# Performance work log

Hardware: AMD Instinct MI355X
Metric: run time of the kernel (lower is better)

Reference implementation:

```python
import jax, jax.numpy as jnp
import numpy as np

B, T, D, H, HD = 2, 2048, 1024, 16, 64
EPS = 1.1920929e-07  # torch.finfo(float32).eps used by F.rms_norm default
VE_GATE_SCALE = 2.0
KEY_OFFSET = True


def rms_norm(x):
    return x * jax.lax.rsqrt(jnp.mean(x * x, axis=-1, keepdims=True) + EPS)


def apply_rotary(x, cos, sin):
    # x: [B,T,H,HD], cos/sin: [T, HD//2]
    c = cos[None, :, None, :]
    s = sin[None, :, None, :]
    x1, x2 = jnp.split(x, 2, axis=-1)
    return jnp.concatenate([x1 * c + x2 * s, -x1 * s + x2 * c], axis=-1)


def setup_inputs() -> dict:
    key = jax.random.key(0)
    ks = jax.random.split(key, 8)
    bound = (3.0 ** 0.5) * (D ** -0.5)
    x = jax.random.normal(ks[0], (B, T, D), dtype=jnp.float32)
    ve = jax.random.normal(ks[1], (B, T, H * HD), dtype=jnp.float32)
    sa_lambdas = jnp.ones((2,), dtype=jnp.float32)
    # realistic RoPE tables
    inv_freq = (10000.0 ** (-np.arange(HD // 2) / (HD // 2))).astype(np.float32)
    ang = np.arange(T, dtype=np.float32)[:, None] * inv_freq[None, :]
    cos = jnp.asarray(np.cos(ang))
    sin = jnp.asarray(np.sin(ang))
    # qkvo weight: uniform init everywhere (orig zeros o-proj; randomized for a non-trivial baseline)
    qkvo_w = jax.random.uniform(ks[2], (4 * D, D), dtype=jnp.float32, minval=-bound, maxval=bound)
    attn_gate_w = 0.02 * jax.random.normal(ks[3], (H, D), dtype=jnp.float32)
    ve_gate_w = 0.02 * jax.random.normal(ks[4], (H, D), dtype=jnp.float32)
    attn_scale = jnp.float32(0.12)
    docs = jnp.sort(jax.random.randint(ks[5], (T,), 0, 8).astype(jnp.int32))
    return {"x": x, "ve": ve, "sa_lambdas": sa_lambdas, "cos": cos, "sin": sin,
            "qkvo_w": qkvo_w, "attn_gate_w": attn_gate_w, "ve_gate_w": ve_gate_w,
            "attn_scale": attn_scale, "docs": docs}


def reference(x, ve, sa_lambdas, cos, sin, qkvo_w, attn_gate_w, ve_gate_w, attn_scale, docs):
    # QKV projection: rows [0:3D] of qkvo_w
    qkv = jnp.einsum('btd,ed->bte', x, sa_lambdas[0] * qkvo_w[:3 * D])
    qkv = qkv.reshape(B, T, 3 * H, HD)
    q, k, v = qkv[:, :, :H], qkv[:, :, H:2 * H], qkv[:, :, 2 * H:]
    q, k = rms_norm(q), rms_norm(k)
    q, k = apply_rotary(q, cos, sin), apply_rotary(k, cos, sin)
    if KEY_OFFSET:
        # shift two head-dim bands of k forward by one position
        k = k.at[:, 1:, :, HD // 4:HD // 2].set(k[:, :-1, :, HD // 4:HD // 2])
        k = k.at[:, 1:, :, 3 * HD // 4:].set(k[:, :-1, :, 3 * HD // 4:])
    # gated value embedding
    ve_gate = VE_GATE_SCALE * jax.nn.sigmoid(jnp.einsum('btd,hd->bth', x, ve_gate_w))
    v = v + ve_gate[..., None] * ve.reshape(B, T, H, HD)
    # causal + document masked attention (score_mod semantics)
    idx = jnp.arange(T)
    mask = (idx[:, None] >= idx[None, :]) & (docs[:, None] == docs[None, :])  # [T,T]
    scores = jnp.einsum('bqhd,bkhd->bhqk', q, k) * attn_scale
    scores = jnp.where(mask[None, None], scores, -jnp.inf)
    p = jax.nn.softmax(scores, axis=-1)
    y = jnp.einsum('bhqk,bkhd->bqhd', p, v)
    # attention output gate
    attn_gate = jax.nn.sigmoid(jnp.einsum('btd,hd->bth', x, attn_gate_w))
    y = y * attn_gate[..., None]
    # output projection: rows [3D:4D]
    y = y.reshape(B, T, H * HD)
    out = jnp.einsum('btd,ed->bte', y, sa_lambdas[1] * qkvo_w[3 * D:])
    return out
```

## Files before the change

### kernel.cpp

```cpp
#include <hip/hip_runtime.h>
#include <math.h>

#define B_ 2
#define T_ 2048
#define D_ 1024
#define H_ 16
#define HD_ 64
#define EPS_ 1.1920929e-07f
#define VE_SCALE_ 2.0f

#define NX4_ (B_ * T_ * D_ / 4)
#define NS4_ (3 * D_ * D_ / 4)
#define NQ4_ (4 * D_ * D_ / 4)
#define NG4_ (H_ * D_ / 4)

typedef __bf16 bf16_t;
typedef __bf16 bf16x4 __attribute__((ext_vector_type(4)));
typedef __bf16 bf16x8 __attribute__((ext_vector_type(8)));
typedef float f32x4 __attribute__((ext_vector_type(4)));

__device__ const f32x4 F4ZERO = {0.f, 0.f, 0.f, 0.f};

typedef __attribute__((address_space(1))) const void gvoid_t;
typedef __attribute__((address_space(3))) void lvoid_t;

__device__ __forceinline__ void gl_lds16(const bf16_t* g, bf16_t* l) {
  __builtin_amdgcn_global_load_lds((gvoid_t*)g, (lvoid_t*)l, 16, 0, 0);
}

__global__ __launch_bounds__(256) void cast_all(
    const float* __restrict__ x, const float* __restrict__ qkvo,
    const float* __restrict__ agw, const float* __restrict__ vgw,
    bf16_t* __restrict__ x_bf, bf16_t* __restrict__ wq,
    bf16_t* __restrict__ wo, bf16_t* __restrict__ wg)
{
  const int i = blockIdx.x * 256 + threadIdx.x;
  const float4* src;
  bf16x4* dst;
  if (i < NX4_) {
    src = (const float4*)x + i;
    dst = (bf16x4*)x_bf + i;
  } else if (i < NX4_ + NS4_) {
    const int j = i - NX4_;
    src = (const float4*)qkvo + j;
    dst = (bf16x4*)wq + j;
  } else if (i < NX4_ + NQ4_) {
    const int j = i - NX4_;
    src = (const float4*)qkvo + j;
    dst = (bf16x4*)wo + (j - NS4_);
  } else if (i < NX4_ + NQ4_ + NG4_) {
    const int j = i - NX4_ - NQ4_;
    src = (const float4*)agw + j;
    dst = (bf16x4*)wg + j;
  } else {
    const int j = i - NX4_ - NQ4_ - NG4_;
    src = (const float4*)vgw + j;
    dst = (bf16x4*)wg + NG4_ + j;
  }
  const float4 v = *src;
  bf16x4 o = {(bf16_t)v.x, (bf16_t)v.y, (bf16_t)v.z, (bf16_t)v.w};
  *dst = o;
}

__global__ __launch_bounds__(256) void gemm_bf16(
    const bf16_t* __restrict__ A, const bf16_t* __restrict__ W,
    void* __restrict__ Cout, int M, int N, int K,
    const float* __restrict__ lam, int li, int out_bf)
{
  const float scale = lam[li];
  __shared__ bf16_t As[2][128][32];
  __shared__ bf16_t Bs[2][128][32];
  const int tid = threadIdx.x;
  const int lane = tid & 63, w = tid >> 6;
  const int lr = lane & 15, lg = lane >> 4;
  const int wr = w >> 1, wc = w & 1;

  const int nwg = gridDim.x * gridDim.y;
  int bid = blockIdx.y * gridDim.x + blockIdx.x;
  bid = (bid & 7) * (nwg >> 3) + (bid >> 3);
  const int row0 = (bid / gridDim.x) * 128;
  const int col0 = (bid % gridDim.x) * 128;

  const int srow = w * 32 + (lane >> 2);
  const int scol = (lane & 3) * 8;
  const bf16_t* Ag = A + (size_t)(row0 + srow) * K + scol;
  const bf16_t* Wg = W + (size_t)(col0 + srow) * K + scol;
  const size_t r16 = (size_t)16 * K;

  f32x4 acc[4][4];
#pragma unroll
  for (int i = 0; i < 4; ++i)
#pragma unroll
    for (int j = 0; j < 4; ++j) acc[i][j] = F4ZERO;

#define STAGE_(bi, kk)                                    \
  do {                                                    \
    gl_lds16(Ag + (kk), &As[bi][w * 32][0]);              \
    gl_lds16(Ag + r16 + (kk), &As[bi][w * 32 + 16][0]);   \
    gl_lds16(Wg + (kk), &Bs[bi][w * 32][0]);              \
    gl_lds16(Wg + r16 + (kk), &Bs[bi][w * 32 + 16][0]);   \
  } while (0)

#define COMPUTE_(bi)                                                     \
  do {                                                                   \
    bf16x8 af[4], bfr[4];                                                \
    _Pragma("unroll")                                                    \
    for (int fm = 0; fm < 4; ++fm)                                       \
      af[fm] = *(const bf16x8*)&As[bi][wr * 64 + fm * 16 + lr][lg * 8];  \
    _Pragma("unroll")                                                    \
    for (int fn = 0; fn < 4; ++fn)                                       \
      bfr[fn] = *(const bf16x8*)&Bs[bi][wc * 64 + fn * 16 + lr][lg * 8]; \
    _Pragma("unroll")                                                    \
    for (int fm = 0; fm < 4; ++fm)                                       \
      _Pragma("unroll")                                                  \
      for (int fn = 0; fn < 4; ++fn)                                     \
        acc[fm][fn] = __builtin_amdgcn_mfma_f32_16x16x32_bf16(           \
            af[fm], bfr[fn], acc[fm][fn], 0, 0, 0);                      \
  } while (0)

  STAGE_(0, 0);
  __syncthreads();
  for (int k0 = 0; k0 + 64 <= K; k0 += 64) {
    STAGE_(1, k0 + 32);
    COMPUTE_(0);
    __syncthreads();
    if (k0 + 64 < K) STAGE_(0, k0 + 64);
    COMPUTE_(1);
    __syncthreads();
  }
#undef STAGE_
#undef COMPUTE_

#pragma unroll
  for (int fm = 0; fm < 4; ++fm)
#pragma unroll
    for (int fn = 0; fn < 4; ++fn)
#pragma unroll
      for (int r = 0; r < 4; ++r) {
        const int row = row0 + wr * 64 + fm * 16 + lg * 4 + r;
        const int col = col0 + wc * 64 + fn * 16 + lr;
        const float v = acc[fm][fn][r] * scale;
        if (out_bf) ((bf16_t*)Cout)[(size_t)row * N + col] = (bf16_t)v;
        else        ((float*)Cout)[(size_t)row * N + col] = v;
      }
}

__global__ __launch_bounds__(256) void post_kernel(
    const float* __restrict__ x, const bf16_t* __restrict__ qkv_b,
    const float* __restrict__ ve, const float* __restrict__ cosb,
    const float* __restrict__ sinb, const bf16_t* __restrict__ wg,
    bf16_t* __restrict__ q_bf, bf16_t* __restrict__ k_bf,
    bf16_t* __restrict__ v_bf, float* __restrict__ attn_gate)
{
  const int bt = blockIdx.x;
  const int b = bt >> 11, t = bt & (T_ - 1);
  const int tid = threadIdx.x;
  __shared__ float xs[D_];
  __shared__ float gsc[32];

  *(float4*)&xs[tid * 4] = ((const float4*)(x + (size_t)bt * D_))[tid];
  __syncthreads();

  {
    const int g = tid >> 3, cg = tid & 7;
    const bf16x8* wrow = (const bf16x8*)(wg + (size_t)g * D_);
    float sum = 0.f;
#pragma unroll
    for (int j = 0; j < 16; ++j) {
      const bf16x8 w8 = wrow[cg + 8 * j];
      const float* xp = &xs[(cg + 8 * j) * 8];
#pragma unroll
      for (int e = 0; e < 8; ++e) sum = fmaf((float)w8[e], xp[e], sum);
    }
    sum += __shfl_xor(sum, 1);
    sum += __shfl_xor(sum, 2);
    sum += __shfl_xor(sum, 4);
    if (cg == 0)
      gsc[g] = (g < 16 ? 1.f : VE_SCALE_) / (1.f + __expf(-sum));
  }
  __syncthreads();

  const int w = tid >> 6, lane = tid & 63;
  const float c = cosb[t * 32 + (lane & 31)];
  const float s = sinb[t * 32 + (lane & 31)];
  const size_t row = (size_t)bt * 3072;
#pragma unroll
  for (int i = 0; i < 4; ++i) {
    const int h = w + i * 4;
    const float qraw = (float)qkv_b[row + h * HD_ + lane];
    const float kraw = (float)qkv_b[row + D_ + h * HD_ + lane];
    const float vraw = (float)qkv_b[row + 2 * D_ + h * HD_ + lane];
    float ssq = qraw * qraw, ssk = kraw * kraw;
#pragma unroll
    for (int off = 32; off > 0; off >>= 1) {
      ssq += __shfl_xor(ssq, off);
      ssk += __shfl_xor(ssk, off);
    }
    const float qn = qraw * rsqrtf(ssq * (1.f / 64.f) + EPS_);
    const float kn = kraw * rsqrtf(ssk * (1.f / 64.f) + EPS_);
    const float qpartner = __shfl_xor(qn, 32);
    const float kpartner = __shfl_xor(kn, 32);
    const float qo = (lane < 32) ? fmaf(qn, c, qpartner * s)
                                 : fmaf(qn, c, -qpartner * s);
    const float ko = (lane < 32) ? fmaf(kn, c, kpartner * s)
                                 : fmaf(kn, c, -kpartner * s);
    const size_t oidx = ((size_t)(b * H_ + h) * T_ + t) * HD_ + lane;
    q_bf[oidx] = (bf16_t)qo;
    k_bf[oidx] = (bf16_t)ko;
    const float vv = fmaf(gsc[16 + h], ve[(size_t)bt * D_ + h * HD_ + lane], vraw);
    v_bf[oidx] = (bf16_t)vv;
    if (lane == 0) attn_gate[bt * H_ + h] = gsc[h];
  }
}

__global__ __launch_bounds__(256) void attn_mfma(
    const bf16_t* __restrict__ q_buf, const bf16_t* __restrict__ k_tmp,
    const bf16_t* __restrict__ v_buf, const float* __restrict__ attn_gate,
    const int* __restrict__ docs, const float* __restrict__ scale_ptr,
    bf16_t* __restrict__ y_buf)
{
  const int qt = blockIdx.x, bh = blockIdx.y;
  const int b = bh >> 4, h = bh & 15;
  const int tid = threadIdx.x;
  const int w = tid >> 6, lane = tid & 63;
  const int lr = lane & 15, lg = lane >> 4;
  const float scale = scale_ptr[0];
  __shared__ bf16_t Ks[64][72];
  __shared__ bf16_t Vt[64][72];
  __shared__ bf16_t Ps[64][72];
  __shared__ int dk[64];

  const int dlo = docs[qt * 64];
  const unsigned long long bal =
      __ballot((lane <= qt) && (docs[lane * 64 + 63] >= dlo));
  const int ktlo = __ffsll(bal) - 1;

  const bf16_t* qp = q_buf + ((size_t)bh * T_ + qt * 64 + w * 16 + lr) * HD_;
  const bf16x8 aq0 = *(const bf16x8*)(qp + lg * 8);
  const bf16x8 aq1 = *(const bf16x8*)(qp + 32 + lg * 8);
  int qpos_r[4], docq_r[4];
#pragma unroll
  for (int r = 0; r < 4; ++r) {
    qpos_r[r] = qt * 64 + w * 16 + lg * 4 + r;
    docq_r[r] = docs[qpos_r[r]];
  }
  f32x4 acc[4];
#pragma unroll
  for (int fn = 0; fn < 4; ++fn) acc[fn] = F4ZERO;
  float m[4] = {-1e30f, -1e30f, -1e30f, -1e30f};
  float l[4] = {0.f, 0.f, 0.f, 0.f};

#pragma unroll 1
  for (int kt = ktlo; kt <= qt; ++kt) {
    __syncthreads();
#pragma unroll
    for (int i = 0; i < 2; ++i) {
      const int idx = i * 256 + tid;
      const int krow = idx >> 3;
      const int c8 = (idx & 7) << 3;
      const int gk = kt * 64 + krow;
      const int gks = (((c8 & 16) != 0) && gk > 0) ? gk - 1 : gk;
      *(bf16x8*)&Ks[krow][c8] =
          *(const bf16x8*)(k_tmp + ((size_t)bh * T_ + gks) * HD_ + c8);
      const int kpos = idx & 63;
      const int d0 = (idx >> 6) << 3;
      const bf16x8 vv =
          *(const bf16x8*)(v_buf + ((size_t)bh * T_ + kt * 64 + kpos) * HD_ + d0);
#pragma unroll
      for (int j = 0; j < 8; ++j) Vt[d0 + j][kpos] = vv[j];
    }
    if (tid < 64) dk[tid] = docs[kt * 64 + tid];
    __syncthreads();

    f32x4 s[4];
#pragma unroll
    for (int fn = 0; fn < 4; ++fn) {
      const bf16x8 bk0 = *(const bf16x8*)&Ks[fn * 16 + lr][lg * 8];
      const bf16x8 bk1 = *(const bf16x8*)&Ks[fn * 16 + lr][32 + lg * 8];
      f32x4 z = F4ZERO;
      z = __builtin_amdgcn_mfma_f32_16x16x32_bf16(aq0, bk0, z, 0, 0, 0);
      s[fn] = __builtin_amdgcn_mfma_f32_16x16x32_bf16(aq1, bk1, z, 0, 0, 0);
    }
    const bool strict = (kt < qt);
#pragma unroll
    for (int fn = 0; fn < 4; ++fn) {
      const int kd = dk[fn * 16 + lr];
      const int kp = kt * 64 + fn * 16 + lr;
#pragma unroll
      for (int r = 0; r < 4; ++r) {
        const bool valid = (kd == docq_r[r]) && (strict || kp <= qpos_r[r]);
        s[fn][r] = valid ? s[fn][r] * scale : -3.0e38f;
      }
    }
#pragma unroll
    for (int r = 0; r < 4; ++r) {
      float cm = fmaxf(fmaxf(s[0][r], s[1][r]), fmaxf(s[2][r], s[3][r]));
      cm = fmaxf(cm, __shfl_xor(cm, 1));
      cm = fmaxf(cm, __shfl_xor(cm, 2));
      cm = fmaxf(cm, __shfl_xor(cm, 4));
      cm = fmaxf(cm, __shfl_xor(cm, 8));
      const float mn = fmaxf(m[r], cm);
      const float sc = __expf(m[r] - mn);
      m[r] = mn;
      const float p0 = __expf(s[0][r] - mn);
      const float p1 = __expf(s[1][r] - mn);
      const float p2 = __expf(s[2][r] - mn);
      const float p3 = __expf(s[3][r] - mn);
      float ps = (p0 + p1) + (p2 + p3);
      ps += __shfl_xor(ps, 1);
      ps += __shfl_xor(ps, 2);
      ps += __shfl_xor(ps, 4);
      ps += __shfl_xor(ps, 8);
      l[r] = l[r] * sc + ps;
      acc[0][r] *= sc; acc[1][r] *= sc; acc[2][r] *= sc; acc[3][r] *= sc;
      const int prow = w * 16 + lg * 4 + r;
      Ps[prow][0 + lr]  = (bf16_t)p0;
      Ps[prow][16 + lr] = (bf16_t)p1;
      Ps[prow][32 + lr] = (bf16_t)p2;
      Ps[prow][48 + lr] = (bf16_t)p3;
    }
    const bf16x8 ap0 = *(const bf16x8*)&Ps[w * 16 + lr][lg * 8];
    const bf16x8 ap1 = *(const bf16x8*)&Ps[w * 16 + lr][32 + lg * 8];
#pragma unroll
    for (int fn = 0; fn < 4; ++fn) {
      const bf16x8 bv0 = *(const bf16x8*)&Vt[fn * 16 + lr][lg * 8];
      const bf16x8 bv1 = *(const bf16x8*)&Vt[fn * 16 + lr][32 + lg * 8];
      acc[fn] = __builtin_amdgcn_mfma_f32_16x16x32_bf16(ap0, bv0, acc[fn], 0, 0, 0);
      acc[fn] = __builtin_amdgcn_mfma_f32_16x16x32_bf16(ap1, bv1, acc[fn], 0, 0, 0);
    }
  }
#pragma unroll
  for (int r = 0; r < 4; ++r) {
    const float inv = attn_gate[(size_t)(b * T_ + qpos_r[r]) * H_ + h] / l[r];
#pragma unroll
    for (int fn = 0; fn < 4; ++fn)
      y_buf[(size_t)(b * T_ + qpos_r[r]) * D_ + h * HD_ + fn * 16 + lr] =
          (bf16_t)(acc[fn][r] * inv);
  }
}

extern "C" void kernel_launch(void* const* d_in, const int* in_sizes, int n_in,
                              void* d_out, int out_size, void* d_ws, size_t ws_size,
                              hipStream_t stream) {
  const float* x    = (const float*)d_in[0];
  const float* ve   = (const float*)d_in[1];
  const float* lam  = (const float*)d_in[2];
  const float* cosb = (const float*)d_in[3];
  const float* sinb = (const float*)d_in[4];
  const float* qkvo = (const float*)d_in[5];
  const float* agw  = (const float*)d_in[6];
  const float* vgw  = (const float*)d_in[7];
  const float* ascl = (const float*)d_in[8];
  const int*   docs = (const int*)d_in[9];
  float* out = (float*)d_out;

  const size_t BT = (size_t)B_ * T_;
  float* cur = (float*)d_ws;
  bf16_t* x_bf = (bf16_t*)cur;        cur += BT * D_ / 2;
  bf16_t* wq_bf = (bf16_t*)cur;       cur += (size_t)3 * D_ * D_ / 2;
  bf16_t* wo_bf = (bf16_t*)cur;       cur += (size_t)D_ * D_ / 2;
  bf16_t* wg_bf = (bf16_t*)cur;       cur += (size_t)2 * H_ * D_ / 2;
  bf16_t* qkv_b = (bf16_t*)cur;       cur += BT * 3 * D_ / 2;
  bf16_t* q_bf = (bf16_t*)cur;        cur += BT * D_ / 2;
  bf16_t* k_bf = (bf16_t*)cur;        cur += BT * D_ / 2;
  bf16_t* v_bf = (bf16_t*)cur;        cur += BT * D_ / 2;
  bf16_t* y_bf = (bf16_t*)cur;        cur += BT * D_ / 2;
  float* attn_gate = cur;             cur += BT * H_;

  cast_all<<<(NX4_ + NQ4_ + 2 * NG4_) / 256, 256, 0, stream>>>(
      x, qkvo, agw, vgw, x_bf, wq_bf, wo_bf, wg_bf);

  gemm_bf16<<<dim3(3 * D_ / 128, BT / 128), 256, 0, stream>>>(
      x_bf, wq_bf, qkv_b, (int)BT, 3 * D_, D_, lam, 0, 1);

  post_kernel<<<(int)BT, 256, 0, stream>>>(
      x, qkv_b, ve, cosb, sinb, wg_bf, q_bf, k_bf, v_bf, attn_gate);

  attn_mfma<<<dim3(T_ / 64, B_ * H_), 256, 0, stream>>>(
      q_bf, k_bf, v_bf, attn_gate, docs, ascl, y_bf);

  gemm_bf16<<<dim3(D_ / 128, BT / 128), 256, 0, stream>>>(
      y_bf, wo_bf, out, (int)BT, D_, D_, lam, 1, 0);
}
```

Before: 131.3 us.

## Add 256x256 tiled bf16 GEMM with phased pipelining for QKV projection

```diff
diff --git a/kernel.cpp b/kernel.cpp
--- a/kernel.cpp
+++ b/kernel.cpp
@@ -62,6 +62,122 @@
   *dst = o;
 }
 
+__global__ __launch_bounds__(512, 2) void gemm256(
+    const bf16_t* __restrict__ A, const bf16_t* __restrict__ W,
+    void* __restrict__ Cout, int M, int N, int K,
+    const float* __restrict__ lam, int li, int out_bf)
+{
+  __shared__ bf16_t As[2][256][64];
+  __shared__ bf16_t Bs[2][256][64];
+  const float scale = lam[li];
+  const int tid = threadIdx.x;
+  const int w = tid >> 6, lane = tid & 63;
+  const int lr = lane & 15, lg = lane >> 4;
+  const int wr = w >> 2, wc = w & 3;
+  const int sw = lr & 7;
+
+  const int nwg = gridDim.x * gridDim.y;
+  int bid = blockIdx.y * gridDim.x + blockIdx.x;
+  bid = (bid & 7) * (nwg >> 3) + (bid >> 3);
+  const int row0 = (bid / gridDim.x) * 256;
+  const int col0 = (bid % gridDim.x) * 256;
+
+  const int arow0 = (w & 3) * 8 + ((w >> 2) ? 128 : 0);
+  const int srow = arow0 + (lane >> 3);
+  const int sgran = (lane & 7) ^ ((lane >> 3) & 7);
+  const bf16_t* Abase = A + (size_t)(row0 + srow) * K + sgran * 8;
+  const bf16_t* Wbase = W + (size_t)(col0 + srow) * K + sgran * 8;
+
+#define STA(buf, j, kk) gl_lds16(Abase + (size_t)((j) * 32) * K + (kk), \
+                                 &As[buf][arow0 + (j) * 32][0])
+#define STB(buf, j, kk) gl_lds16(Wbase + (size_t)((j) * 32) * K + (kk), \
+                                 &Bs[buf][arow0 + (j) * 32][0])
+#define LDA(buf, fm, kh) \
+  (*(const bf16x8*)&As[buf][wr * 128 + (fm) * 16 + lr][((((kh) * 4) + lg) ^ sw) * 8])
+#define LDB(buf, fn, kh) \
+  (*(const bf16x8*)&Bs[buf][wc * 64 + (fn) * 16 + lr][((((kh) * 4) + lg) ^ sw) * 8])
+
+  f32x4 acc[8][4];
+#pragma unroll
+  for (int i = 0; i < 8; ++i)
+#pragma unroll
+    for (int j = 0; j < 4; ++j) acc[i][j] = F4ZERO;
+  bf16x8 bb[4][2];
+
+#define PH(vm, q, cur, ISSUE)                                                  \
+  do {                                                                         \
+    asm volatile("s_waitcnt vmcnt(" #vm ")" ::: "memory");                     \
+    __builtin_amdgcn_s_barrier();                                              \
+    if ((q) == 0) {                                                            \
+      _Pragma("unroll") for (int fn = 0; fn < 4; ++fn) {                       \
+        bb[fn][0] = LDB(cur, fn, 0);                                           \
+        bb[fn][1] = LDB(cur, fn, 1);                                           \
+      }                                                                        \
+    }                                                                          \
+    bf16x8 a00 = LDA(cur, 2 * (q), 0), a01 = LDA(cur, 2 * (q), 1);             \
+    bf16x8 a10 = LDA(cur, 2 * (q) + 1, 0), a11 = LDA(cur, 2 * (q) + 1, 1);     \
+    ISSUE;                                                                     \
+    asm volatile("s_waitcnt lgkmcnt(0)" ::: "memory");                         \
+    __builtin_amdgcn_sched_barrier(0);                                         \
+    __builtin_amdgcn_s_setprio(1);                                             \
+    _Pragma("unroll") for (int fn = 0; fn < 4; ++fn) {                         \
+      acc[2 * (q)][fn] = __builtin_amdgcn_mfma_f32_16x16x32_bf16(              \
+          a00, bb[fn][0], acc[2 * (q)][fn], 0, 0, 0);                          \
+      acc[2 * (q)][fn] = __builtin_amdgcn_mfma_f32_16x16x32_bf16(              \
+          a01, bb[fn][1], acc[2 * (q)][fn], 0, 0, 0);                          \
+      acc[2 * (q) + 1][fn] = __builtin_amdgcn_mfma_f32_16x16x32_bf16(          \
+          a10, bb[fn][0], acc[2 * (q) + 1][fn], 0, 0, 0);                      \
+      acc[2 * (q) + 1][fn] = __builtin_amdgcn_mfma_f32_16x16x32_bf16(          \
+          a11, bb[fn][1], acc[2 * (q) + 1][fn], 0, 0, 0);                      \
+    }                                                                          \
+    __builtin_amdgcn_s_setprio(0);                                             \
+    __builtin_amdgcn_s_barrier();                                              \
+  } while (0)
+
+  STB(0, 0, 0); STB(0, 1, 0); STB(0, 2, 0); STB(0, 3, 0);
+  STA(0, 0, 0); STA(0, 1, 0); STA(0, 2, 0); STA(0, 3, 0);
+
+  const int nt = K >> 6;
+  int kt = 0;
+  for (; kt < nt - 1; ++kt) {
+    const int kn = (kt + 1) << 6;
+    if ((kt & 1) == 0) {
+      PH(3, 0, 0, { STB(1, 0, kn); STB(1, 1, kn); });
+      PH(4, 1, 0, { STB(1, 2, kn); STB(1, 3, kn); });
+      PH(5, 2, 0, { STA(1, 0, kn); STA(1, 1, kn); });
+      PH(6, 3, 0, { STA(1, 2, kn); STA(1, 3, kn); });
+    } else {
+      PH(3, 0, 1, { STB(0, 0, kn); STB(0, 1, kn); });
+      PH(4, 1, 1, { STB(0, 2, kn); STB(0, 3, kn); });
+      PH(5, 2, 1, { STA(0, 0, kn); STA(0, 1, kn); });
+      PH(6, 3, 1, { STA(0, 2, kn); STA(0, 3, kn); });
+    }
+  }
+  if ((kt & 1) == 0) {
+    PH(3, 0, 0, {}); PH(2, 1, 0, {}); PH(1, 2, 0, {}); PH(0, 3, 0, {});
+  } else {
+    PH(3, 0, 1, {}); PH(2, 1, 1, {}); PH(1, 2, 1, {}); PH(0, 3, 1, {});
+  }
+#undef PH
+#undef STA
+#undef STB
+#undef LDA
+#undef LDB
+
+#pragma unroll
+  for (int fm = 0; fm < 8; ++fm)
+#pragma unroll
+    for (int fn = 0; fn < 4; ++fn)
+#pragma unroll
+      for (int r = 0; r < 4; ++r) {
+        const int row = row0 + wr * 128 + fm * 16 + lg * 4 + r;
+        const int col = col0 + wc * 64 + fn * 16 + lr;
+        const float v = acc[fm][fn][r] * scale;
+        if (out_bf) ((bf16_t*)Cout)[(size_t)row * N + col] = (bf16_t)v;
+        else        ((float*)Cout)[(size_t)row * N + col] = v;
+      }
+}
+
 __global__ __launch_bounds__(256) void gemm_bf16(
     const bf16_t* __restrict__ A, const bf16_t* __restrict__ W,
     void* __restrict__ Cout, int M, int N, int K,
@@ -146,7 +262,7 @@
 }
 
 __global__ __launch_bounds__(256) void post_kernel(
-    const float* __restrict__ x, const bf16_t* __restrict__ qkv_b,
+    const bf16_t* __restrict__ x_bf, const bf16_t* __restrict__ qkv_b,
     const float* __restrict__ ve, const float* __restrict__ cosb,
     const float* __restrict__ sinb, const bf16_t* __restrict__ wg,
     bf16_t* __restrict__ q_bf, bf16_t* __restrict__ k_bf,
@@ -158,7 +274,13 @@
   __shared__ float xs[D_];
   __shared__ float gsc[32];
 
-  *(float4*)&xs[tid * 4] = ((const float4*)(x + (size_t)bt * D_))[tid];
+  {
+    const bf16x4 xv = ((const bf16x4*)(x_bf + (size_t)bt * D_))[tid];
+    xs[tid * 4 + 0] = (float)xv[0];
+    xs[tid * 4 + 1] = (float)xv[1];
+    xs[tid * 4 + 2] = (float)xv[2];
+    xs[tid * 4 + 3] = (float)xv[3];
+  }
   __syncthreads();
 
   {
@@ -370,11 +492,11 @@
   cast_all<<<(NX4_ + NQ4_ + 2 * NG4_) / 256, 256, 0, stream>>>(
       x, qkvo, agw, vgw, x_bf, wq_bf, wo_bf, wg_bf);
 
-  gemm_bf16<<<dim3(3 * D_ / 128, BT / 128), 256, 0, stream>>>(
+  gemm256<<<dim3(3 * D_ / 256, BT / 256), 512, 0, stream>>>(
       x_bf, wq_bf, qkv_b, (int)BT, 3 * D_, D_, lam, 0, 1);
 
   post_kernel<<<(int)BT, 256, 0, stream>>>(
-      x, qkv_b, ve, cosb, sinb, wg_bf, q_bf, k_bf, v_bf, attn_gate);
+      x_bf, qkv_b, ve, cosb, sinb, wg_bf, q_bf, k_bf, v_bf, attn_gate);
 
   attn_mfma<<<dim3(T_ / 64, B_ * H_), 256, 0, stream>>>(
       q_bf, k_bf, v_bf, attn_gate, docs, ascl, y_bf);
```

New measurement: 276.3 us. 110% more time.

## Split-K the output projection with atomics and read bf16 x in post kernel

Applied to the files above, without the earlier changes.

```diff
diff --git a/kernel.cpp b/kernel.cpp
--- a/kernel.cpp
+++ b/kernel.cpp
@@ -32,9 +32,16 @@
     const float* __restrict__ x, const float* __restrict__ qkvo,
     const float* __restrict__ agw, const float* __restrict__ vgw,
     bf16_t* __restrict__ x_bf, bf16_t* __restrict__ wq,
-    bf16_t* __restrict__ wo, bf16_t* __restrict__ wg)
+    bf16_t* __restrict__ wo, bf16_t* __restrict__ wg,
+    float* __restrict__ outz)
 {
   const int i = blockIdx.x * 256 + threadIdx.x;
+  if (i >= NX4_ + NQ4_ + 2 * NG4_) {
+    const int j = i - (NX4_ + NQ4_ + 2 * NG4_);
+    float4 z; z.x = 0.f; z.y = 0.f; z.z = 0.f; z.w = 0.f;
+    ((float4*)outz)[j] = z;
+    return;
+  }
   const float4* src;
   bf16x4* dst;
   if (i < NX4_) {
@@ -75,6 +82,10 @@
   const int lr = lane & 15, lg = lane >> 4;
   const int wr = w >> 1, wc = w & 1;
 
+  const int kparts = gridDim.z;
+  const int Keff = K / kparts;
+  const int koff = blockIdx.z * Keff;
+
   const int nwg = gridDim.x * gridDim.y;
   int bid = blockIdx.y * gridDim.x + blockIdx.x;
   bid = (bid & 7) * (nwg >> 3) + (bid >> 3);
@@ -83,8 +94,8 @@
 
   const int srow = w * 32 + (lane >> 2);
   const int scol = (lane & 3) * 8;
-  const bf16_t* Ag = A + (size_t)(row0 + srow) * K + scol;
-  const bf16_t* Wg = W + (size_t)(col0 + srow) * K + scol;
+  const bf16_t* Ag = A + (size_t)(row0 + srow) * K + koff + scol;
+  const bf16_t* Wg = W + (size_t)(col0 + srow) * K + koff + scol;
   const size_t r16 = (size_t)16 * K;
 
   f32x4 acc[4][4];
@@ -120,11 +131,11 @@
 
   STAGE_(0, 0);
   __syncthreads();
-  for (int k0 = 0; k0 + 64 <= K; k0 += 64) {
+  for (int k0 = 0; k0 + 64 <= Keff; k0 += 64) {
     STAGE_(1, k0 + 32);
     COMPUTE_(0);
     __syncthreads();
-    if (k0 + 64 < K) STAGE_(0, k0 + 64);
+    if (k0 + 64 < Keff) STAGE_(0, k0 + 64);
     COMPUTE_(1);
     __syncthreads();
   }
@@ -140,13 +151,17 @@
         const int row = row0 + wr * 64 + fm * 16 + lg * 4 + r;
         const int col = col0 + wc * 64 + fn * 16 + lr;
         const float v = acc[fm][fn][r] * scale;
-        if (out_bf) ((bf16_t*)Cout)[(size_t)row * N + col] = (bf16_t)v;
-        else        ((float*)Cout)[(size_t)row * N + col] = v;
+        if (kparts > 1)
+          unsafeAtomicAdd(&((float*)Cout)[(size_t)row * N + col], v);
+        else if (out_bf)
+          ((bf16_t*)Cout)[(size_t)row * N + col] = (bf16_t)v;
+        else
+          ((float*)Cout)[(size_t)row * N + col] = v;
       }
 }
 
 __global__ __launch_bounds__(256) void post_kernel(
-    const float* __restrict__ x, const bf16_t* __restrict__ qkv_b,
+    const bf16_t* __restrict__ x_bf, const bf16_t* __restrict__ qkv_b,
     const float* __restrict__ ve, const float* __restrict__ cosb,
     const float* __restrict__ sinb, const bf16_t* __restrict__ wg,
     bf16_t* __restrict__ q_bf, bf16_t* __restrict__ k_bf,
@@ -158,7 +173,13 @@
   __shared__ float xs[D_];
   __shared__ float gsc[32];
 
-  *(float4*)&xs[tid * 4] = ((const float4*)(x + (size_t)bt * D_))[tid];
+  {
+    const bf16x4 xv = ((const bf16x4*)(x_bf + (size_t)bt * D_))[tid];
+    xs[tid * 4 + 0] = (float)xv[0];
+    xs[tid * 4 + 1] = (float)xv[1];
+    xs[tid * 4 + 2] = (float)xv[2];
+    xs[tid * 4 + 3] = (float)xv[3];
+  }
   __syncthreads();
 
   {
@@ -367,18 +388,18 @@
   bf16_t* y_bf = (bf16_t*)cur;        cur += BT * D_ / 2;
   float* attn_gate = cur;             cur += BT * H_;
 
-  cast_all<<<(NX4_ + NQ4_ + 2 * NG4_) / 256, 256, 0, stream>>>(
-      x, qkvo, agw, vgw, x_bf, wq_bf, wo_bf, wg_bf);
+  cast_all<<<(2 * NX4_ + NQ4_ + 2 * NG4_) / 256, 256, 0, stream>>>(
+      x, qkvo, agw, vgw, x_bf, wq_bf, wo_bf, wg_bf, out);
 
   gemm_bf16<<<dim3(3 * D_ / 128, BT / 128), 256, 0, stream>>>(
       x_bf, wq_bf, qkv_b, (int)BT, 3 * D_, D_, lam, 0, 1);
 
   post_kernel<<<(int)BT, 256, 0, stream>>>(
-      x, qkv_b, ve, cosb, sinb, wg_bf, q_bf, k_bf, v_bf, attn_gate);
+      x_bf, qkv_b, ve, cosb, sinb, wg_bf, q_bf, k_bf, v_bf, attn_gate);
 
   attn_mfma<<<dim3(T_ / 64, B_ * H_), 256, 0, stream>>>(
       q_bf, k_bf, v_bf, attn_gate, docs, ascl, y_bf);
 
-  gemm_bf16<<<dim3(D_ / 128, BT / 128), 256, 0, stream>>>(
+  gemm_bf16<<<dim3(D_ / 128, BT / 128, 2), 256, 0, stream>>>(
       y_bf, wo_bf, out, (int)BT, D_, D_, lam, 1, 0);
 }
```

After: 146.2 us. 11.3% more time.

## Fuse RMS norm, RoPE and value-gate epilogue into QKV GEMM

Applied to the files above, without the earlier changes.

```diff
diff --git a/kernel.cpp b/kernel.cpp
--- a/kernel.cpp
+++ b/kernel.cpp
@@ -62,10 +62,165 @@
   *dst = o;
 }
 
+__global__ __launch_bounds__(256) void gates_kernel(
+    const bf16_t* __restrict__ x_bf, const bf16_t* __restrict__ wg,
+    float* __restrict__ attn_gate, float* __restrict__ ve_gate2)
+{
+  const int bt = blockIdx.x;
+  const int tid = threadIdx.x;
+  __shared__ float xs[D_];
+  {
+    const bf16x4 xv = ((const bf16x4*)(x_bf + (size_t)bt * D_))[tid];
+    xs[tid * 4 + 0] = (float)xv[0];
+    xs[tid * 4 + 1] = (float)xv[1];
+    xs[tid * 4 + 2] = (float)xv[2];
+    xs[tid * 4 + 3] = (float)xv[3];
+  }
+  __syncthreads();
+  const int g = tid >> 3, cg = tid & 7;
+  const bf16x8* wrow = (const bf16x8*)(wg + (size_t)g * D_);
+  float sum = 0.f;
+#pragma unroll
+  for (int j = 0; j < 16; ++j) {
+    const bf16x8 w8 = wrow[cg + 8 * j];
+    const float* xp = &xs[(cg + 8 * j) * 8];
+#pragma unroll
+    for (int e = 0; e < 8; ++e) sum = fmaf((float)w8[e], xp[e], sum);
+  }
+  sum += __shfl_xor(sum, 1);
+  sum += __shfl_xor(sum, 2);
+  sum += __shfl_xor(sum, 4);
+  if (cg == 0) {
+    const float sg = 1.f / (1.f + __expf(-sum));
+    if (g < 16) attn_gate[bt * H_ + g] = sg;
+    else        ve_gate2[bt * H_ + (g - 16)] = VE_SCALE_ * sg;
+  }
+}
+
+__global__ __launch_bounds__(256) void gemm_qkv(
+    const bf16_t* __restrict__ A, const bf16_t* __restrict__ W,
+    const float* __restrict__ ve, const float* __restrict__ cosb,
+    const float* __restrict__ sinb, const float* __restrict__ ve_gate2,
+    bf16_t* __restrict__ q_bf, bf16_t* __restrict__ k_bf,
+    bf16_t* __restrict__ v_bf, int K,
+    const float* __restrict__ lam)
+{
+  const float scale = lam[0];
+  __shared__ bf16_t As[2][128][32];
+  __shared__ bf16_t Bs[2][128][32];
+  const int tid = threadIdx.x;
+  const int lane = tid & 63, w = tid >> 6;
+  const int lr = lane & 15, lg = lane >> 4;
+  const int wr = w >> 1, wc = w & 1;
+
+  const int nwg = gridDim.x * gridDim.y;
+  int bid = blockIdx.y * gridDim.x + blockIdx.x;
+  bid = (bid & 7) * (nwg >> 3) + (bid >> 3);
+  const int row0 = (bid / gridDim.x) * 128;
+  const int col0 = (bid % gridDim.x) * 128;
+
+  const int srow = w * 32 + (lane >> 2);
+  const int scol = (lane & 3) * 8;
+  const bf16_t* Ag = A + (size_t)(row0 + srow) * K + scol;
+  const bf16_t* Wg = W + (size_t)(col0 + srow) * K + scol;
+  const size_t r16 = (size_t)16 * K;
+
+  f32x4 acc[4][4];
+#pragma unroll
+  for (int i = 0; i < 4; ++i)
+#pragma unroll
+    for (int j = 0; j < 4; ++j) acc[i][j] = F4ZERO;
+
+#define STAGE_(bi, kk)                                    \
+  do {                                                    \
+    gl_lds16(Ag + (kk), &As[bi][w * 32][0]);              \
+    gl_lds16(Ag + r16 + (kk), &As[bi][w * 32 + 16][0]);   \
+    gl_lds16(Wg + (kk), &Bs[bi][w * 32][0]);              \
+    gl_lds16(Wg + r16 + (kk), &Bs[bi][w * 32 + 16][0]);   \
+  } while (0)
+
+#define COMPUTE_(bi)                                                     \
+  do {                                                                   \
+    bf16x8 af[4], bfr[4];                                                \
+    _Pragma("unroll")                                                    \
+    for (int fm = 0; fm < 4; ++fm)                                       \
+      af[fm] = *(const bf16x8*)&As[bi][wr * 64 + fm * 16 + lr][lg * 8];  \
+    _Pragma("unroll")                                                    \
+    for (int fn = 0; fn < 4; ++fn)                                       \
+      bfr[fn] = *(const bf16x8*)&Bs[bi][wc * 64 + fn * 16 + lr][lg * 8]; \
+    _Pragma("unroll")                                                    \
+    for (int fm = 0; fm < 4; ++fm)                                       \
+      _Pragma("unroll")                                                  \
+      for (int fn = 0; fn < 4; ++fn)                                     \
+        acc[fm][fn] = __builtin_amdgcn_mfma_f32_16x16x32_bf16(           \
+            af[fm], bfr[fn], acc[fm][fn], 0, 0, 0);                      \
+  } while (0)
+
+  STAGE_(0, 0);
+  __syncthreads();
+  for (int k0 = 0; k0 + 64 <= K; k0 += 64) {
+    STAGE_(1, k0 + 32);
+    COMPUTE_(0);
+    __syncthreads();
+    if (k0 + 64 < K) STAGE_(0, k0 + 64);
+    COMPUTE_(1);
+    __syncthreads();
+  }
+#undef STAGE_
+#undef COMPUTE_
+
+  const int sec = col0 >> 10;
+  const int h = ((col0 & 1023) >> 6) + wc;
+#pragma unroll
+  for (int fm = 0; fm < 4; ++fm) {
+#pragma unroll
+    for (int r = 0; r < 4; ++r) {
+      const int row = row0 + wr * 64 + fm * 16 + lg * 4 + r;
+      const int b = row >> 11, t = row & (T_ - 1);
+      float v0 = acc[fm][0][r] * scale;
+      float v1 = acc[fm][1][r] * scale;
+      float v2 = acc[fm][2][r] * scale;
+      float v3 = acc[fm][3][r] * scale;
+      const size_t obase = ((size_t)(b * H_ + h) * T_ + t) * HD_;
+      if (sec < 2) {
+        float ssq = v0 * v0 + v1 * v1 + v2 * v2 + v3 * v3;
+        ssq += __shfl_xor(ssq, 1);
+        ssq += __shfl_xor(ssq, 2);
+        ssq += __shfl_xor(ssq, 4);
+        ssq += __shfl_xor(ssq, 8);
+        const float rn = rsqrtf(ssq * (1.f / 64.f) + EPS_);
+        v0 *= rn; v1 *= rn; v2 *= rn; v3 *= rn;
+        const float c0 = cosb[t * 32 + lr], s0 = sinb[t * 32 + lr];
+        const float c1 = cosb[t * 32 + 16 + lr], s1 = sinb[t * 32 + 16 + lr];
+        const float o0 = fmaf(v0, c0, v2 * s0);
+        const float o2 = fmaf(v2, c0, -v0 * s0);
+        const float o1 = fmaf(v1, c1, v3 * s1);
+        const float o3 = fmaf(v3, c1, -v1 * s1);
+        bf16_t* dst = (sec == 0 ? q_bf : k_bf);
+        dst[obase + 0 + lr]  = (bf16_t)o0;
+        dst[obase + 16 + lr] = (bf16_t)o1;
+        dst[obase + 32 + lr] = (bf16_t)o2;
+        dst[obase + 48 + lr] = (bf16_t)o3;
+      } else {
+        const float g = ve_gate2[row * H_ + h];
+        const float* vp = ve + (size_t)row * D_ + h * HD_;
+        v0 = fmaf(g, vp[0 + lr], v0);
+        v1 = fmaf(g, vp[16 + lr], v1);
+        v2 = fmaf(g, vp[32 + lr], v2);
+        v3 = fmaf(g, vp[48 + lr], v3);
+        v_bf[obase + 0 + lr]  = (bf16_t)v0;
+        v_bf[obase + 16 + lr] = (bf16_t)v1;
+        v_bf[obase + 32 + lr] = (bf16_t)v2;
+        v_bf[obase + 48 + lr] = (bf16_t)v3;
+      }
+    }
+  }
+}
+
 __global__ __launch_bounds__(256) void gemm_bf16(
     const bf16_t* __restrict__ A, const bf16_t* __restrict__ W,
-    void* __restrict__ Cout, int M, int N, int K,
-    const float* __restrict__ lam, int li, int out_bf)
+    float* __restrict__ Cout, int M, int N, int K,
+    const float* __restrict__ lam, int li)
 {
   const float scale = lam[li];
   __shared__ bf16_t As[2][128][32];
@@ -139,78 +294,8 @@
       for (int r = 0; r < 4; ++r) {
         const int row = row0 + wr * 64 + fm * 16 + lg * 4 + r;
         const int col = col0 + wc * 64 + fn * 16 + lr;
-        const float v = acc[fm][fn][r] * scale;
-        if (out_bf) ((bf16_t*)Cout)[(size_t)row * N + col] = (bf16_t)v;
-        else        ((float*)Cout)[(size_t)row * N + col] = v;
+        Cout[(size_t)row * N + col] = acc[fm][fn][r] * scale;
       }
-}
-
-__global__ __launch_bounds__(256) void post_kernel(
-    const float* __restrict__ x, const bf16_t* __restrict__ qkv_b,
-    const float* __restrict__ ve, const float* __restrict__ cosb,
-    const float* __restrict__ sinb, const bf16_t* __restrict__ wg,
-    bf16_t* __restrict__ q_bf, bf16_t* __restrict__ k_bf,
-    bf16_t* __restrict__ v_bf, float* __restrict__ attn_gate)
-{
-  const int bt = blockIdx.x;
-  const int b = bt >> 11, t = bt & (T_ - 1);
-  const int tid = threadIdx.x;
-  __shared__ float xs[D_];
-  __shared__ float gsc[32];
-
-  *(float4*)&xs[tid * 4] = ((const float4*)(x + (size_t)bt * D_))[tid];
-  __syncthreads();
-
-  {
-    const int g = tid >> 3, cg = tid & 7;
-    const bf16x8* wrow = (const bf16x8*)(wg + (size_t)g * D_);
-    float sum = 0.f;
-#pragma unroll
-    for (int j = 0; j < 16; ++j) {
-      const bf16x8 w8 = wrow[cg + 8 * j];
-      const float* xp = &xs[(cg + 8 * j) * 8];
-#pragma unroll
-      for (int e = 0; e < 8; ++e) sum = fmaf((float)w8[e], xp[e], sum);
-    }
-    sum += __shfl_xor(sum, 1);
-    sum += __shfl_xor(sum, 2);
-    sum += __shfl_xor(sum, 4);
-    if (cg == 0)
-      gsc[g] = (g < 16 ? 1.f : VE_SCALE_) / (1.f + __expf(-sum));
-  }
-  __syncthreads();
-
-  const int w = tid >> 6, lane = tid & 63;
-  const float c = cosb[t * 32 + (lane & 31)];
-  const float s = sinb[t * 32 + (lane & 31)];
-  const size_t row = (size_t)bt * 3072;
-#pragma unroll
-  for (int i = 0; i < 4; ++i) {
-    const int h = w + i * 4;
-    const float qraw = (float)qkv_b[row + h * HD_ + lane];
-    const float kraw = (float)qkv_b[row + D_ + h * HD_ + lane];
-    const float vraw = (float)qkv_b[row + 2 * D_ + h * HD_ + lane];
-    float ssq = qraw * qraw, ssk = kraw * kraw;
-#pragma unroll
-    for (int off = 32; off > 0; off >>= 1) {
-      ssq += __shfl_xor(ssq, off);
-      ssk += __shfl_xor(ssk, off);
-    }
-    const float qn = qraw * rsqrtf(ssq * (1.f / 64.f) + EPS_);
-    const float kn = kraw * rsqrtf(ssk * (1.f / 64.f) + EPS_);
-    const float qpartner = __shfl_xor(qn, 32);
-    const float kpartner = __shfl_xor(kn, 32);
-    const float qo = (lane < 32) ? fmaf(qn, c, qpartner * s)
-                                 : fmaf(qn, c, -qpartner * s);
-    const float ko = (lane < 32) ? fmaf(kn, c, kpartner * s)
-                                 : fmaf(kn, c, -kpartner * s);
-    const size_t oidx = ((size_t)(b * H_ + h) * T_ + t) * HD_ + lane;
-    q_bf[oidx] = (bf16_t)qo;
-    k_bf[oidx] = (bf16_t)ko;
-    const float vv = fmaf(gsc[16 + h], ve[(size_t)bt * D_ + h * HD_ + lane], vraw);
-    v_bf[oidx] = (bf16_t)vv;
-    if (lane == 0) attn_gate[bt * H_ + h] = gsc[h];
-  }
 }
 
 __global__ __launch_bounds__(256) void attn_mfma(
@@ -360,25 +445,24 @@
   bf16_t* wq_bf = (bf16_t*)cur;       cur += (size_t)3 * D_ * D_ / 2;
   bf16_t* wo_bf = (bf16_t*)cur;       cur += (size_t)D_ * D_ / 2;
   bf16_t* wg_bf = (bf16_t*)cur;       cur += (size_t)2 * H_ * D_ / 2;
-  bf16_t* qkv_b = (bf16_t*)cur;       cur += BT * 3 * D_ / 2;
   bf16_t* q_bf = (bf16_t*)cur;        cur += BT * D_ / 2;
   bf16_t* k_bf = (bf16_t*)cur;        cur += BT * D_ / 2;
   bf16_t* v_bf = (bf16_t*)cur;        cur += BT * D_ / 2;
   bf16_t* y_bf = (bf16_t*)cur;        cur += BT * D_ / 2;
   float* attn_gate = cur;             cur += BT * H_;
+  float* ve_gate2 = cur;              cur += BT * H_;
 
   cast_all<<<(NX4_ + NQ4_ + 2 * NG4_) / 256, 256, 0, stream>>>(
       x, qkvo, agw, vgw, x_bf, wq_bf, wo_bf, wg_bf);
 
-  gemm_bf16<<<dim3(3 * D_ / 128, BT / 128), 256, 0, stream>>>(
-      x_bf, wq_bf, qkv_b, (int)BT, 3 * D_, D_, lam, 0, 1);
-
-  post_kernel<<<(int)BT, 256, 0, stream>>>(
-      x, qkv_b, ve, cosb, sinb, wg_bf, q_bf, k_bf, v_bf, attn_gate);
+  gates_kernel<<<(int)BT, 256, 0, stream>>>(x_bf, wg_bf, attn_gate, ve_gate2);
+
+  gemm_qkv<<<dim3(3 * D_ / 128, BT / 128), 256, 0, stream>>>(
+      x_bf, wq_bf, ve, cosb, sinb, ve_gate2, q_bf, k_bf, v_bf, D_, lam);
 
   attn_mfma<<<dim3(T_ / 64, B_ * H_), 256, 0, stream>>>(
       q_bf, k_bf, v_bf, attn_gate, docs, ascl, y_bf);
 
   gemm_bf16<<<dim3(D_ / 128, BT / 128), 256, 0, stream>>>(
-      y_bf, wo_bf, out, (int)BT, D_, D_, lam, 1, 0);
-}
+      y_bf, wo_bf, out, (int)BT, D_, D_, lam, 1);
+}
```

Measured after the change: 121.6 us. 1.08x faster.
